# Kernel optimization log

Measured on AMD Instinct MI355X. Metric: run time of the kernel, lower is better.

The kernel has to match this reference:

```python
import jax, jax.numpy as jnp
import numpy as np

EMB = 512
HEAD = 64
B, S = 4, 4096


def setup_inputs() -> dict:
    key = jax.random.key(0)
    kq, kk, kv, kwq, kwk, kwv = jax.random.split(key, 6)
    q = jax.random.normal(kq, (B, S, EMB), dtype=jnp.float32)
    k = jax.random.normal(kk, (B, S, EMB), dtype=jnp.float32)
    v = jax.random.normal(kv, (B, S, EMB), dtype=jnp.float32)
    # nn.Linear weights: [out_features, in_features], no bias
    sc = 1.0 / np.sqrt(EMB)
    Wq = jax.random.uniform(kwq, (HEAD, EMB), jnp.float32, -sc, sc)
    Wk = jax.random.uniform(kwk, (HEAD, EMB), jnp.float32, -sc, sc)
    Wv = jax.random.uniform(kwv, (HEAD, EMB), jnp.float32, -sc, sc)
    return {"q": q, "k": k, "v": v, "Wq": Wq, "Wk": Wk, "Wv": Wv}


def reference(q, k, v, Wq, Wk, Wv):
    scale = 1.0 / np.sqrt(HEAD).astype(np.float32)
    Q = jnp.einsum('bse,he->bsh', q, Wq)  # [B,S,HEAD]
    K = jnp.einsum('bse,he->bsh', k, Wk)
    V = jnp.einsum('bse,he->bsh', v, Wv)
    scores = jnp.einsum('bqh,bkh->bqk', Q, K) * scale  # [B,S,S]
    attn = jax.nn.softmax(scores, axis=-1)
    # dropout p=0.0 -> identity
    out = jnp.einsum('bqk,bkh->bqh', attn, V)  # [B,S,HEAD]
    return out
```

## Files before the change

### kernel.cpp

```cpp
#include <hip/hip_runtime.h>
#include <hip/hip_bf16.h>

#define EMB    512
#define HEAD   64
#define SEQ    4096
#define NB     4
#define NSPLIT 8
#define LDX    72

#define SL2E   0.18033688011112042f

typedef __bf16 bf16x8 __attribute__((ext_vector_type(8)));
typedef float  f32x4  __attribute__((ext_vector_type(4)));

__device__ inline ushort4 cvt4(float4 v) {
    __hip_bfloat16 a = __float2bfloat16(v.x), b = __float2bfloat16(v.y);
    __hip_bfloat16 c = __float2bfloat16(v.z), d = __float2bfloat16(v.w);
    ushort4 r;
    r.x = *(unsigned short*)&a; r.y = *(unsigned short*)&b;
    r.z = *(unsigned short*)&c; r.w = *(unsigned short*)&d;
    return r;
}

__global__ __launch_bounds__(256) void cvtw_kernel(
    const float* __restrict__ Wq, const float* __restrict__ Wk,
    const float* __restrict__ Wv, __hip_bfloat16* __restrict__ Wc)
{
    int idx   = blockIdx.x * 256 + threadIdx.x;
    int which = idx >> 13;
    int off   = (idx & 8191) * 4;
    const float* src = (which == 0) ? Wq : (which == 1) ? Wk : Wv;
    float s = (which == 0) ? SL2E : 1.0f;
    float4 v = *(const float4*)(src + off);
    v.x *= s; v.y *= s; v.z *= s; v.w *= s;
    *(ushort4*)(Wc + which * 64 * EMB + off) = cvt4(v);
}

__global__ __launch_bounds__(256) void proj_kernel(
    const float* __restrict__ q, const float* __restrict__ k, const float* __restrict__ v,
    const __hip_bfloat16* __restrict__ Wc,
    __hip_bfloat16* __restrict__ Qo, __hip_bfloat16* __restrict__ Ko,
    __hip_bfloat16* __restrict__ Vto)
{
    __shared__ __hip_bfloat16 Xs[32][LDX];

    const int which = blockIdx.y;
    const float* __restrict__ x = (which == 0) ? q : (which == 1) ? k : v;
    const __hip_bfloat16* __restrict__ W = Wc + which * 64 * EMB;

    const int tid  = threadIdx.x;
    const int wave = tid >> 6, lane = tid & 63;
    const int l16  = lane & 15, quad = lane >> 4;
    const int rs   = (wave & 1) * 16;
    const int ch   = wave >> 1;
    const int r0   = blockIdx.x * 32;
    const float* __restrict__ xb = x + (size_t)r0 * EMB;

    const int sr = tid >> 4;
    const int sc = (tid & 15) << 2;

    const f32x4 z = {0.f, 0.f, 0.f, 0.f};
    f32x4 acc[2] = {z, z};

    float4 xr[2];
    bf16x8 wf[4];

#define LOADX(dst, e0)                                                        \
    _Pragma("unroll")                                                         \
    for (int it = 0; it < 2; ++it)                                            \
        dst[it] = *(const float4*)(xb + (size_t)(it * 16 + sr) * EMB + (e0) + sc);

#define LOADW(dst, e0)                                                        \
    _Pragma("unroll")                                                         \
    for (int st = 0; st < 2; ++st)                                            \
        _Pragma("unroll")                                                     \
        for (int tt = 0; tt < 2; ++tt)                                        \
            dst[st * 2 + tt] = *(const bf16x8*)(W + (size_t)((ch * 2 + tt) * 16 + l16) * EMB \
                                                + (e0) + st * 32 + quad * 8);

    LOADX(xr, 0);
    LOADW(wf, 0);

    #pragma unroll
    for (int c = 0; c < 8; ++c) {
        const int e0 = c * 64;
        if (c) __syncthreads();
        #pragma unroll
        for (int it = 0; it < 2; ++it)
            *(ushort4*)&Xs[it * 16 + sr][sc] = cvt4(xr[it]);
        __syncthreads();

        bf16x8 a0 = *(const bf16x8*)&Xs[rs + l16][quad * 8];
        bf16x8 a1 = *(const bf16x8*)&Xs[rs + l16][32 + quad * 8];

        float4 xr2[2];
        bf16x8 wf2[4];
        if (c < 7) { LOADX(xr2, e0 + 64); LOADW(wf2, e0 + 64); }

        #pragma unroll
        for (int tt = 0; tt < 2; ++tt)
            acc[tt] = __builtin_amdgcn_mfma_f32_16x16x32_bf16(a0, wf[tt], acc[tt], 0, 0, 0);
        #pragma unroll
        for (int tt = 0; tt < 2; ++tt)
            acc[tt] = __builtin_amdgcn_mfma_f32_16x16x32_bf16(a1, wf[2 + tt], acc[tt], 0, 0, 0);

        if (c < 7) {
            #pragma unroll
            for (int it = 0; it < 2; ++it) xr[it] = xr2[it];
            #pragma unroll
            for (int j = 0; j < 4; ++j) wf[j] = wf2[j];
        }
    }
#undef LOADX
#undef LOADW

    #pragma unroll
    for (int tt = 0; tt < 2; ++tt) {
        #pragma unroll
        for (int r = 0; r < 4; ++r) {
            int row = r0 + rs + quad * 4 + r;
            int h   = (ch * 2 + tt) * 16 + l16;
            __hip_bfloat16 val = __float2bfloat16(acc[tt][r]);
            if (which == 0) {
                Qo[(size_t)row * HEAD + h] = val;
            } else if (which == 1) {
                Ko[(size_t)row * HEAD + h] = val;
            } else {
                int b = row >> 12, s = row & (SEQ - 1);
                Vto[((size_t)b * HEAD + h) * SEQ + s] = val;
            }
        }
    }
}

__global__ __launch_bounds__(256) void attn_kernel(
    const __hip_bfloat16* __restrict__ Qb, const __hip_bfloat16* __restrict__ Kb,
    const __hip_bfloat16* __restrict__ Vt, float* __restrict__ Op,
    float* __restrict__ lp)
{
    __shared__ __hip_bfloat16 Ks[64][LDX];
    __shared__ __hip_bfloat16 Vs[64][LDX];
    __shared__ __hip_bfloat16 Ps[128][LDX];

    const int tid  = threadIdx.x;
    const int wave = tid >> 6, lane = tid & 63;
    const int l16  = lane & 15, quad = lane >> 4;
    const int b    = blockIdx.y;
    const int q0   = blockIdx.x * 128;
    const int j0b  = blockIdx.z * (SEQ / NSPLIT);

    bf16x8 qf[2][2];
    #pragma unroll
    for (int s = 0; s < 2; ++s) {
        const __hip_bfloat16* qrow =
            Qb + ((size_t)b * SEQ + q0 + wave * 32 + s * 16 + l16) * HEAD + quad * 8;
        qf[s][0] = *(const bf16x8*)(qrow);
        qf[s][1] = *(const bf16x8*)(qrow + 32);
    }

    const f32x4 z = {0.f, 0.f, 0.f, 0.f};
    f32x4 oacc[2][4] = {{z, z, z, z}, {z, z, z, z}};
    f32x4 lacc[2] = {z, z};

    const __hip_bfloat16 one_bf = __float2bfloat16(1.0f);
    bf16x8 ones;
    #pragma unroll
    for (int j = 0; j < 8; ++j) ones[j] = *(const __bf16*)&one_bf;

    for (int jt = 0; jt < SEQ / NSPLIT; jt += 64) {
        const int j0 = j0b + jt;
        __syncthreads();
        for (int i = tid; i < 512; i += 256) {
            int r = i >> 3, c8 = (i & 7) * 8;
            *(uint4*)&Ks[r][c8] =
                *(const uint4*)(Kb + ((size_t)b * SEQ + j0 + r) * HEAD + c8);
            *(uint4*)&Vs[r][c8] =
                *(const uint4*)(Vt + ((size_t)b * HEAD + r) * SEQ + j0 + c8);
        }
        __syncthreads();

        f32x4 sacc[2][4] = {{z, z, z, z}, {z, z, z, z}};
        #pragma unroll
        for (int st = 0; st < 2; ++st) {
            #pragma unroll
            for (int t = 0; t < 4; ++t) {
                bf16x8 kf = *(const bf16x8*)&Ks[t * 16 + l16][st * 32 + quad * 8];
                #pragma unroll
                for (int s = 0; s < 2; ++s)
                    sacc[s][t] = __builtin_amdgcn_mfma_f32_16x16x32_bf16(qf[s][st], kf, sacc[s][t], 0, 0, 0);
            }
        }

        #pragma unroll
        for (int s = 0; s < 2; ++s)
            #pragma unroll
            for (int r = 0; r < 4; ++r)
                #pragma unroll
                for (int t = 0; t < 4; ++t) {
                    float p = __builtin_amdgcn_exp2f(sacc[s][t][r]);
                    Ps[wave * 32 + s * 16 + quad * 4 + r][t * 16 + l16] = __float2bfloat16(p);
                }

        #pragma unroll
        for (int s = 0; s < 2; ++s) {
            #pragma unroll
            for (int st = 0; st < 2; ++st) {
                bf16x8 pf = *(const bf16x8*)&Ps[wave * 32 + s * 16 + l16][st * 32 + quad * 8];
                lacc[s] = __builtin_amdgcn_mfma_f32_16x16x32_bf16(pf, ones, lacc[s], 0, 0, 0);
                #pragma unroll
                for (int t = 0; t < 4; ++t) {
                    bf16x8 vf = *(const bf16x8*)&Vs[t * 16 + l16][st * 32 + quad * 8];
                    oacc[s][t] = __builtin_amdgcn_mfma_f32_16x16x32_bf16(pf, vf, oacc[s][t], 0, 0, 0);
                }
            }
        }
    }

    const size_t pb = (size_t)(blockIdx.z * NB + b) * SEQ;
    #pragma unroll
    for (int s = 0; s < 2; ++s) {
        const size_t row0 = pb + q0 + wave * 32 + s * 16 + quad * 4;
        if (l16 == 0) {
            #pragma unroll
            for (int r = 0; r < 4; ++r)
                lp[row0 + r] = lacc[s][r];
        }
        #pragma unroll
        for (int t = 0; t < 4; ++t)
            #pragma unroll
            for (int r = 0; r < 4; ++r)
                Op[(row0 + r) * HEAD + t * 16 + l16] = oacc[s][t][r];
    }
}

__global__ __launch_bounds__(256) void merge_kernel(
    const float* __restrict__ Op, const float* __restrict__ lp,
    float* __restrict__ out)
{
    int idx = blockIdx.x * 256 + threadIdx.x;
    int bq  = idx >> 4;
    int c4  = (idx & 15) * 4;
    float4 acc = {0.f, 0.f, 0.f, 0.f};
    float  l   = 0.f;
    #pragma unroll
    for (int s = 0; s < NSPLIT; ++s) {
        float4 o = *(const float4*)(Op + ((size_t)s * NB * SEQ + bq) * HEAD + c4);
        acc.x += o.x; acc.y += o.y; acc.z += o.z; acc.w += o.w;
        l += lp[(size_t)s * NB * SEQ + bq];
    }
    float inv = 1.f / l;
    float4 r = {acc.x * inv, acc.y * inv, acc.z * inv, acc.w * inv};
    *(float4*)(out + (size_t)bq * HEAD + c4) = r;
}

extern "C" void kernel_launch(void* const* d_in, const int* in_sizes, int n_in,
                              void* d_out, int out_size, void* d_ws, size_t ws_size,
                              hipStream_t stream) {
    const float* q  = (const float*)d_in[0];
    const float* k  = (const float*)d_in[1];
    const float* v  = (const float*)d_in[2];
    const float* Wq = (const float*)d_in[3];
    const float* Wk = (const float*)d_in[4];
    const float* Wv = (const float*)d_in[5];
    float* out = (float*)d_out;

    __hip_bfloat16* Qb = (__hip_bfloat16*)d_ws;
    __hip_bfloat16* Kb = Qb + (size_t)NB * SEQ * HEAD;
    __hip_bfloat16* Vt = Kb + (size_t)NB * SEQ * HEAD;
    __hip_bfloat16* Wc = Vt + (size_t)NB * SEQ * HEAD;
    float* Op = (float*)(Wc + 3 * 64 * EMB);
    float* lp = Op + (size_t)NSPLIT * NB * SEQ * HEAD;

    cvtw_kernel<<<96, 256, 0, stream>>>(Wq, Wk, Wv, Wc);

    dim3 pgrid(NB * SEQ / 32, 3);
    proj_kernel<<<pgrid, dim3(256), 0, stream>>>(q, k, v, Wc, Qb, Kb, Vt);

    dim3 agrid(SEQ / 128, NB, NSPLIT);
    attn_kernel<<<agrid, dim3(256), 0, stream>>>(Qb, Kb, Vt, Op, lp);

    merge_kernel<<<(NB * SEQ * 16) / 256, dim3(256), 0, stream>>>(Op, lp, out);
}
```

Measured before the change: 180.2 us.

## Double per-block query tile, prefetch K/V into registers, vectorize P stores

Each attention block now covers 256 query rows, 64 per wave, so every K/V tile loaded into shared memory is reused by twice as many queries. The next K/V tile is prefetched into registers while the current tile is computed, and the K/V fragments are hoisted out of the inner loops. The score MFMA operands are swapped so the transposed scores can be written to shared memory as 4-wide vector stores, with the P buffer shrunk to 16 rows per wave and reused. The trade-off is higher register pressure and only half as many blocks, which could reduce occupancy and latency hiding.

```diff
diff --git a/kernel.cpp b/kernel.cpp
--- a/kernel.cpp
+++ b/kernel.cpp
@@ -133,93 +133,111 @@
     }
 }
 
-__global__ __launch_bounds__(256) void attn_kernel(
+__global__ __launch_bounds__(256, 2) void attn_kernel(
     const __hip_bfloat16* __restrict__ Qb, const __hip_bfloat16* __restrict__ Kb,
     const __hip_bfloat16* __restrict__ Vt, float* __restrict__ Op,
     float* __restrict__ lp)
 {
     __shared__ __hip_bfloat16 Ks[64][LDX];
     __shared__ __hip_bfloat16 Vs[64][LDX];
-    __shared__ __hip_bfloat16 Ps[128][LDX];
+    __shared__ __hip_bfloat16 Ps[64][LDX];
 
     const int tid  = threadIdx.x;
     const int wave = tid >> 6, lane = tid & 63;
     const int l16  = lane & 15, quad = lane >> 4;
     const int b    = blockIdx.y;
-    const int q0   = blockIdx.x * 128;
+    const int q0   = blockIdx.x * 256;
     const int j0b  = blockIdx.z * (SEQ / NSPLIT);
-
-    bf16x8 qf[2][2];
-    #pragma unroll
-    for (int s = 0; s < 2; ++s) {
+    const int NT   = SEQ / NSPLIT / 64;
+
+    bf16x8 qf[4][2];
+    #pragma unroll
+    for (int s = 0; s < 4; ++s) {
         const __hip_bfloat16* qrow =
-            Qb + ((size_t)b * SEQ + q0 + wave * 32 + s * 16 + l16) * HEAD + quad * 8;
+            Qb + ((size_t)b * SEQ + q0 + wave * 64 + s * 16 + l16) * HEAD + quad * 8;
         qf[s][0] = *(const bf16x8*)(qrow);
         qf[s][1] = *(const bf16x8*)(qrow + 32);
     }
 
     const f32x4 z = {0.f, 0.f, 0.f, 0.f};
-    f32x4 oacc[2][4] = {{z, z, z, z}, {z, z, z, z}};
-    f32x4 lacc[2] = {z, z};
+    f32x4 oacc[4][4] = {{z, z, z, z}, {z, z, z, z}, {z, z, z, z}, {z, z, z, z}};
+    f32x4 lacc[4] = {z, z, z, z};
 
     const __hip_bfloat16 one_bf = __float2bfloat16(1.0f);
     bf16x8 ones;
     #pragma unroll
     for (int j = 0; j < 8; ++j) ones[j] = *(const __bf16*)&one_bf;
 
-    for (int jt = 0; jt < SEQ / NSPLIT; jt += 64) {
-        const int j0 = j0b + jt;
+    const int sr0 = tid >> 3;
+    const int sc8 = (tid & 7) * 8;
+
+#define STAGE_LOAD(kr, vr, j0)                                                \
+    _Pragma("unroll")                                                         \
+    for (int it = 0; it < 2; ++it) {                                          \
+        int r = sr0 + it * 32;                                                \
+        kr[it] = *(const uint4*)(Kb + ((size_t)b * SEQ + (j0) + r) * HEAD + sc8); \
+        vr[it] = *(const uint4*)(Vt + ((size_t)b * HEAD + r) * SEQ + (j0) + sc8); \
+    }
+
+    uint4 kr[2], vr[2];
+    STAGE_LOAD(kr, vr, j0b);
+
+    for (int jt = 0; jt < NT; ++jt) {
         __syncthreads();
-        for (int i = tid; i < 512; i += 256) {
-            int r = i >> 3, c8 = (i & 7) * 8;
-            *(uint4*)&Ks[r][c8] =
-                *(const uint4*)(Kb + ((size_t)b * SEQ + j0 + r) * HEAD + c8);
-            *(uint4*)&Vs[r][c8] =
-                *(const uint4*)(Vt + ((size_t)b * HEAD + r) * SEQ + j0 + c8);
+        #pragma unroll
+        for (int it = 0; it < 2; ++it) {
+            int r = sr0 + it * 32;
+            *(uint4*)&Ks[r][sc8] = kr[it];
+            *(uint4*)&Vs[r][sc8] = vr[it];
         }
         __syncthreads();
 
-        f32x4 sacc[2][4] = {{z, z, z, z}, {z, z, z, z}};
-        #pragma unroll
-        for (int st = 0; st < 2; ++st) {
+        if (jt + 1 < NT) { STAGE_LOAD(kr, vr, j0b + (jt + 1) * 64); }
+
+        bf16x8 kf[2][4], vf[2][4];
+        #pragma unroll
+        for (int st = 0; st < 2; ++st)
             #pragma unroll
             for (int t = 0; t < 4; ++t) {
-                bf16x8 kf = *(const bf16x8*)&Ks[t * 16 + l16][st * 32 + quad * 8];
+                kf[st][t] = *(const bf16x8*)&Ks[t * 16 + l16][st * 32 + quad * 8];
+                vf[st][t] = *(const bf16x8*)&Vs[t * 16 + l16][st * 32 + quad * 8];
+            }
+
+        #pragma unroll
+        for (int s = 0; s < 4; ++s) {
+            f32x4 sacc[4] = {z, z, z, z};
+            #pragma unroll
+            for (int st = 0; st < 2; ++st)
                 #pragma unroll
-                for (int s = 0; s < 2; ++s)
-                    sacc[s][t] = __builtin_amdgcn_mfma_f32_16x16x32_bf16(qf[s][st], kf, sacc[s][t], 0, 0, 0);
+                for (int t = 0; t < 4; ++t)
+                    sacc[t] = __builtin_amdgcn_mfma_f32_16x16x32_bf16(kf[st][t], qf[s][st], sacc[t], 0, 0, 0);
+
+            #pragma unroll
+            for (int t = 0; t < 4; ++t) {
+                float4 p;
+                p.x = __builtin_amdgcn_exp2f(sacc[t][0]);
+                p.y = __builtin_amdgcn_exp2f(sacc[t][1]);
+                p.z = __builtin_amdgcn_exp2f(sacc[t][2]);
+                p.w = __builtin_amdgcn_exp2f(sacc[t][3]);
+                *(ushort4*)&Ps[wave * 16 + l16][t * 16 + quad * 4] = cvt4(p);
             }
-        }
-
-        #pragma unroll
-        for (int s = 0; s < 2; ++s)
-            #pragma unroll
-            for (int r = 0; r < 4; ++r)
-                #pragma unroll
-                for (int t = 0; t < 4; ++t) {
-                    float p = __builtin_amdgcn_exp2f(sacc[s][t][r]);
-                    Ps[wave * 32 + s * 16 + quad * 4 + r][t * 16 + l16] = __float2bfloat16(p);
-                }
-
-        #pragma unroll
-        for (int s = 0; s < 2; ++s) {
+
             #pragma unroll
             for (int st = 0; st < 2; ++st) {
-                bf16x8 pf = *(const bf16x8*)&Ps[wave * 32 + s * 16 + l16][st * 32 + quad * 8];
+                bf16x8 pf = *(const bf16x8*)&Ps[wave * 16 + l16][st * 32 + quad * 8];
                 lacc[s] = __builtin_amdgcn_mfma_f32_16x16x32_bf16(pf, ones, lacc[s], 0, 0, 0);
                 #pragma unroll
-                for (int t = 0; t < 4; ++t) {
-                    bf16x8 vf = *(const bf16x8*)&Vs[t * 16 + l16][st * 32 + quad * 8];
-                    oacc[s][t] = __builtin_amdgcn_mfma_f32_16x16x32_bf16(pf, vf, oacc[s][t], 0, 0, 0);
-                }
+                for (int t = 0; t < 4; ++t)
+                    oacc[s][t] = __builtin_amdgcn_mfma_f32_16x16x32_bf16(pf, vf[st][t], oacc[s][t], 0, 0, 0);
             }
         }
     }
+#undef STAGE_LOAD
 
     const size_t pb = (size_t)(blockIdx.z * NB + b) * SEQ;
     #pragma unroll
-    for (int s = 0; s < 2; ++s) {
-        const size_t row0 = pb + q0 + wave * 32 + s * 16 + quad * 4;
+    for (int s = 0; s < 4; ++s) {
+        const size_t row0 = pb + q0 + wave * 64 + s * 16 + quad * 4;
         if (l16 == 0) {
             #pragma unroll
             for (int r = 0; r < 4; ++r)
@@ -276,7 +294,7 @@
     dim3 pgrid(NB * SEQ / 32, 3);
     proj_kernel<<<pgrid, dim3(256), 0, stream>>>(q, k, v, Wc, Qb, Kb, Vt);
 
-    dim3 agrid(SEQ / 128, NB, NSPLIT);
+    dim3 agrid(SEQ / 256, NB, NSPLIT);
     attn_kernel<<<agrid, dim3(256), 0, stream>>>(Qb, Kb, Vt, Op, lp);
 
     merge_kernel<<<(NB * SEQ * 16) / 256, dim3(256), 0, stream>>>(Op, lp, out);
```

Result: no change. 179.6 us (-0.3%).
